# Kernel optimization log

Measured on AMD Instinct MI355X. Metric: run time of the kernel, lower is better.

## Reference

```python
import jax, jax.numpy as jnp
import numpy as np

N_PARTICLES = 262144
N_PAIRS = 8388608
DENSITY = 0.8
BOX_L = float((N_PARTICLES / DENSITY) ** (1.0 / 3.0))  # ~68.8


def setup_inputs() -> dict:
    key = jax.random.key(0)
    k_x, k_i, k_j = jax.random.split(key, 3)
    # positions uniform in the periodic box [0, L)^3
    x = jax.random.uniform(k_x, (N_PARTICLES, 3), dtype=jnp.float32) * BOX_L
    idx_i = jax.random.randint(k_i, (N_PAIRS,), 0, N_PARTICLES, dtype=jnp.int32)
    idx_j = jax.random.randint(k_j, (N_PAIRS,), 0, N_PARTICLES, dtype=jnp.int32)
    # avoid self-pairs (r2 == 0) the real neighbor list excludes (dists > 1e-6)
    idx_j = jnp.where(idx_j == idx_i, (idx_j + 1) % N_PARTICLES, idx_j)
    eps = jnp.float32(1.0)
    sigma = jnp.float32(1.0)
    box_size = jnp.full((3,), BOX_L, dtype=jnp.float32)
    return {"x": x, "eps": eps, "sigma": sigma, "box_size": box_size,
            "idx_i": idx_i, "idx_j": idx_j}


def reference(x, eps, sigma, box_size, idx_i, idx_j):
    # neighbor-list gather: (n_pairs, 3)
    diff = x[idx_i] - x[idx_j]
    # minimum image convention: wrap to [-L/2, L/2]
    diff = diff - box_size * jnp.round(diff / box_size)
    r2 = jnp.sum(diff * diff, axis=-1)          # (n_pairs,)
    s2 = (sigma * sigma) / r2
    s6 = s2 * s2 * s2
    u_pairs = 4.0 * eps * (s6 * s6 - s6)
    return jnp.sum(u_pairs)
```

## Files before the change

kernel.cpp:

```cpp
#include <hip/hip_runtime.h>


__global__ __launch_bounds__(256) void lj_pairs_kernel(
    const float* __restrict__ x,
    const float* __restrict__ eps_p,
    const float* __restrict__ sig_p,
    const float* __restrict__ box_p,
    const int4*  __restrict__ idx_i4,
    const int4*  __restrict__ idx_j4,
    double*      __restrict__ acc)
{
    const int t = blockIdx.x * blockDim.x + threadIdx.x;

    const float eps  = eps_p[0];
    const float sig  = sig_p[0];
    const float sig2 = sig * sig;
    const float L0 = box_p[0], L1 = box_p[1], L2 = box_p[2];
    const float i0 = 1.0f / L0, i1 = 1.0f / L1, i2 = 1.0f / L2;

    const int4 ii = idx_i4[t];
    const int4 jj = idx_j4[t];
    const int ia[4] = {ii.x, ii.y, ii.z, ii.w};
    const int ja[4] = {jj.x, jj.y, jj.z, jj.w};

    float sum = 0.0f;
#pragma unroll
    for (int k = 0; k < 4; ++k) {
        const float* pi = x + 3 * ia[k];
        const float* pj = x + 3 * ja[k];
        float dx = pi[0] - pj[0];
        float dy = pi[1] - pj[1];
        float dz = pi[2] - pj[2];
        dx -= L0 * rintf(dx * i0);
        dy -= L1 * rintf(dy * i1);
        dz -= L2 * rintf(dz * i2);
        const float r2 = dx * dx + dy * dy + dz * dz;
        const float s2 = sig2 / r2;
        const float s6 = s2 * s2 * s2;
        sum += s6 * s6 - s6;
    }
    double dsum = (double)(4.0f * eps * sum);

    #pragma unroll
    for (int off = 32; off > 0; off >>= 1)
        dsum += __shfl_down(dsum, off, 64);

    __shared__ double wsum[4];
    const int lane = threadIdx.x & 63;
    const int wave = threadIdx.x >> 6;
    if (lane == 0) wsum[wave] = dsum;
    __syncthreads();
    if (threadIdx.x == 0) {
        const double b = wsum[0] + wsum[1] + wsum[2] + wsum[3];
        atomicAdd(acc, b);
    }
}

__global__ void lj_finalize_kernel(const double* __restrict__ acc,
                                   float* __restrict__ out)
{
    out[0] = (float)acc[0];
}

extern "C" void kernel_launch(void* const* d_in, const int* in_sizes, int n_in,
                              void* d_out, int out_size, void* d_ws, size_t ws_size,
                              hipStream_t stream) {
    const float* x     = (const float*)d_in[0];
    const float* eps   = (const float*)d_in[1];
    const float* sigma = (const float*)d_in[2];
    const float* box   = (const float*)d_in[3];
    const int4*  ii    = (const int4*)d_in[4];
    const int4*  jj    = (const int4*)d_in[5];
    float* out = (float*)d_out;
    double* acc = (double*)d_ws;

    const int n_pairs = in_sizes[4];
    const int threads_total = n_pairs / 4;
    const int block = 256;
    const int grid = threads_total / block;

    hipMemsetAsync(acc, 0, sizeof(double), stream);
    lj_pairs_kernel<<<grid, block, 0, stream>>>(x, eps, sigma, box, ii, jj, acc);
    lj_finalize_kernel<<<1, 1, 0, stream>>>(acc, out);
}
```

Baseline: 201.7 us.

## Repack positions to float4, stream index loads, replace atomics with partial reduction

Adds a repack kernel that copies the xyz positions into a 16-byte padded float4 array, so each random gather is one vector load instead of three scalar loads. Index arrays are read with nontemporal loads so they do not displace the position data from cache. The per-block atomicAdd into one double is replaced by per-block partial sums and a single-block final reduction kernel. This costs an extra kernel launch and a 4 MB workspace write per call, and falls back to the unpacked path when the workspace is too small.

```diff
diff --git a/kernel.cpp b/kernel.cpp
--- a/kernel.cpp
+++ b/kernel.cpp
@@ -1,14 +1,28 @@
 #include <hip/hip_runtime.h>
 
 
-__global__ __launch_bounds__(256) void lj_pairs_kernel(
-    const float* __restrict__ x,
+typedef int  vint4  __attribute__((ext_vector_type(4)));
+
+__global__ __launch_bounds__(256) void repack_kernel(
+    const float* __restrict__ x, float* __restrict__ xp, int n3)
+{
+    int t = blockIdx.x * 256 + threadIdx.x;
+    if (t < n3) {
+        float v = x[t];
+        int p = t / 3;
+        int c = t - 3 * p;
+        xp[4 * p + c] = v;
+    }
+}
+
+__global__ __launch_bounds__(256) void lj_pairs4_kernel(
+    const float4* __restrict__ xp,
     const float* __restrict__ eps_p,
     const float* __restrict__ sig_p,
     const float* __restrict__ box_p,
-    const int4*  __restrict__ idx_i4,
-    const int4*  __restrict__ idx_j4,
-    double*      __restrict__ acc)
+    const vint4* __restrict__ idx_i4,
+    const vint4* __restrict__ idx_j4,
+    double*      __restrict__ partial)
 {
     const int t = blockIdx.x * blockDim.x + threadIdx.x;
 
@@ -18,8 +32,58 @@
     const float L0 = box_p[0], L1 = box_p[1], L2 = box_p[2];
     const float i0 = 1.0f / L0, i1 = 1.0f / L1, i2 = 1.0f / L2;
 
-    const int4 ii = idx_i4[t];
-    const int4 jj = idx_j4[t];
+    const vint4 ii = __builtin_nontemporal_load(idx_i4 + t);
+    const vint4 jj = __builtin_nontemporal_load(idx_j4 + t);
+    const int ia[4] = {ii.x, ii.y, ii.z, ii.w};
+    const int ja[4] = {jj.x, jj.y, jj.z, jj.w};
+
+    float sum = 0.0f;
+#pragma unroll
+    for (int k = 0; k < 4; ++k) {
+        const float4 pi = xp[ia[k]];
+        const float4 pj = xp[ja[k]];
+        float dx = pi.x - pj.x;
+        float dy = pi.y - pj.y;
+        float dz = pi.z - pj.z;
+        dx -= L0 * rintf(dx * i0);
+        dy -= L1 * rintf(dy * i1);
+        dz -= L2 * rintf(dz * i2);
+        const float r2 = dx * dx + dy * dy + dz * dz;
+        const float s2 = sig2 / r2;
+        const float s6 = s2 * s2 * s2;
+        sum += s6 * s6 - s6;
+    }
+    double dsum = (double)(4.0f * eps * sum);
+
+    #pragma unroll
+    for (int off = 32; off > 0; off >>= 1)
+        dsum += __shfl_down(dsum, off, 64);
+
+    __shared__ double wsum[4];
+    if ((threadIdx.x & 63) == 0) wsum[threadIdx.x >> 6] = dsum;
+    __syncthreads();
+    if (threadIdx.x == 0)
+        partial[blockIdx.x] = wsum[0] + wsum[1] + wsum[2] + wsum[3];
+}
+
+__global__ __launch_bounds__(256) void lj_pairs3_kernel(
+    const float* __restrict__ x,
+    const float* __restrict__ eps_p,
+    const float* __restrict__ sig_p,
+    const float* __restrict__ box_p,
+    const vint4* __restrict__ idx_i4,
+    const vint4* __restrict__ idx_j4,
+    double*      __restrict__ partial)
+{
+    const int t = blockIdx.x * blockDim.x + threadIdx.x;
+    const float eps  = eps_p[0];
+    const float sig  = sig_p[0];
+    const float sig2 = sig * sig;
+    const float L0 = box_p[0], L1 = box_p[1], L2 = box_p[2];
+    const float i0 = 1.0f / L0, i1 = 1.0f / L1, i2 = 1.0f / L2;
+
+    const vint4 ii = __builtin_nontemporal_load(idx_i4 + t);
+    const vint4 jj = __builtin_nontemporal_load(idx_j4 + t);
     const int ia[4] = {ii.x, ii.y, ii.z, ii.w};
     const int ja[4] = {jj.x, jj.y, jj.z, jj.w};
 
@@ -40,26 +104,30 @@
         sum += s6 * s6 - s6;
     }
     double dsum = (double)(4.0f * eps * sum);
-
     #pragma unroll
     for (int off = 32; off > 0; off >>= 1)
         dsum += __shfl_down(dsum, off, 64);
-
     __shared__ double wsum[4];
-    const int lane = threadIdx.x & 63;
-    const int wave = threadIdx.x >> 6;
-    if (lane == 0) wsum[wave] = dsum;
+    if ((threadIdx.x & 63) == 0) wsum[threadIdx.x >> 6] = dsum;
     __syncthreads();
-    if (threadIdx.x == 0) {
-        const double b = wsum[0] + wsum[1] + wsum[2] + wsum[3];
-        atomicAdd(acc, b);
-    }
+    if (threadIdx.x == 0)
+        partial[blockIdx.x] = wsum[0] + wsum[1] + wsum[2] + wsum[3];
 }
 
-__global__ void lj_finalize_kernel(const double* __restrict__ acc,
-                                   float* __restrict__ out)
+__global__ __launch_bounds__(256) void reduce_kernel(
+    const double* __restrict__ partial, int n, float* __restrict__ out)
 {
-    out[0] = (float)acc[0];
+    double s = 0.0;
+    for (int i = threadIdx.x; i < n; i += 256)
+        s += partial[i];
+    #pragma unroll
+    for (int off = 32; off > 0; off >>= 1)
+        s += __shfl_down(s, off, 64);
+    __shared__ double wsum[4];
+    if ((threadIdx.x & 63) == 0) wsum[threadIdx.x >> 6] = s;
+    __syncthreads();
+    if (threadIdx.x == 0)
+        out[0] = (float)(wsum[0] + wsum[1] + wsum[2] + wsum[3]);
 }
 
 extern "C" void kernel_launch(void* const* d_in, const int* in_sizes, int n_in,
@@ -69,17 +137,28 @@
     const float* eps   = (const float*)d_in[1];
     const float* sigma = (const float*)d_in[2];
     const float* box   = (const float*)d_in[3];
-    const int4*  ii    = (const int4*)d_in[4];
-    const int4*  jj    = (const int4*)d_in[5];
+    const vint4* ii    = (const vint4*)d_in[4];
+    const vint4* jj    = (const vint4*)d_in[5];
     float* out = (float*)d_out;
-    double* acc = (double*)d_ws;
 
     const int n_pairs = in_sizes[4];
-    const int threads_total = n_pairs / 4;
+    const int n_part  = in_sizes[0] / 3;
     const int block = 256;
-    const int grid = threads_total / block;
+    const int grid = (n_pairs / 4) / block;
 
-    hipMemsetAsync(acc, 0, sizeof(double), stream);
-    lj_pairs_kernel<<<grid, block, 0, stream>>>(x, eps, sigma, box, ii, jj, acc);
-    lj_finalize_kernel<<<1, 1, 0, stream>>>(acc, out);
+    const size_t packed_bytes = (size_t)n_part * 16;
+    const size_t partial_bytes = (size_t)grid * sizeof(double);
+
+    if (ws_size >= packed_bytes + partial_bytes) {
+        float4* xp = (float4*)d_ws;
+        double* partial = (double*)((char*)d_ws + packed_bytes);
+        const int n3 = n_part * 3;
+        repack_kernel<<<(n3 + block - 1) / block, block, 0, stream>>>(x, (float*)xp, n3);
+        lj_pairs4_kernel<<<grid, block, 0, stream>>>(xp, eps, sigma, box, ii, jj, partial);
+        reduce_kernel<<<1, block, 0, stream>>>(partial, grid, out);
+    } else {
+        double* partial = (double*)d_ws;
+        lj_pairs3_kernel<<<grid, block, 0, stream>>>(x, eps, sigma, box, ii, jj, partial);
+        reduce_kernel<<<1, block, 0, stream>>>(partial, grid, out);
+    }
 }
```

Measured after the change: 193.4 us. -4.1%, faster.
